# Optimization experiments

Measured on AMD Instinct MI355X. Metric: run time of the kernel, lower is better.

The kernel has to match this reference:

```python
import jax, jax.numpy as jnp
import numpy as np

D_MODEL = 1024
N_HEADS = 16
N_KV_HEADS = 4
HEAD_DIM = 64


def setup_inputs() -> dict:
    key = jax.random.key(0)
    ks = jax.random.split(key, 5)
    B, T, P = 2, 512, 8
    scale = 1.0 / np.sqrt(D_MODEL)
    return {
        "hidden_states": jax.random.normal(ks[0], (B, T, P, D_MODEL), dtype=jnp.float32),
        # weights stored [in, out] so y = x @ W (same math as nn.Linear with W^T)
        "Wq": jax.random.normal(ks[1], (D_MODEL, N_HEADS * HEAD_DIM), dtype=jnp.float32) * scale,
        "Wk": jax.random.normal(ks[2], (D_MODEL, N_KV_HEADS * HEAD_DIM), dtype=jnp.float32) * scale,
        "Wv": jax.random.normal(ks[3], (D_MODEL, N_KV_HEADS * HEAD_DIM), dtype=jnp.float32) * scale,
        "Wo": jax.random.normal(ks[4], (N_HEADS * HEAD_DIM, D_MODEL), dtype=jnp.float32) * scale,
    }


def _rope_tables(T, d):
    half = d // 2
    inv_freq = 1.0 / (10000.0 ** (jnp.arange(half, dtype=jnp.float32) / half))
    pos = jnp.arange(T, dtype=jnp.float32)
    angles = pos[:, None] * inv_freq[None, :]  # (T, half)
    return jnp.cos(angles), jnp.sin(angles)


def _apply_rope(x, cos, sin):
    # x: (B, P, T, H, d); cos/sin: (T, d/2)
    half = x.shape[-1] // 2
    x1, x2 = x[..., :half], x[..., half:]
    c = cos[None, None, :, None, :]
    s = sin[None, None, :, None, :]
    return jnp.concatenate([x1 * c - x2 * s, x1 * s + x2 * c], axis=-1)


def reference(hidden_states, Wq, Wk, Wv, Wo):
    B, T, P, _ = hidden_states.shape
    x = jnp.transpose(hidden_states, (0, 2, 1, 3))  # (B, P, T, C)
    q = (x @ Wq).reshape(B, P, T, N_HEADS, HEAD_DIM)
    k = (x @ Wk).reshape(B, P, T, N_KV_HEADS, HEAD_DIM)
    v = (x @ Wv).reshape(B, P, T, N_KV_HEADS, HEAD_DIM)

    rep = N_HEADS // N_KV_HEADS
    k = jnp.repeat(k, rep, axis=3)  # (B,P,T,H,d) interleaved like torch repeat/view
    v = jnp.repeat(v, rep, axis=3)

    cos, sin = _rope_tables(T, HEAD_DIM)
    q = _apply_rope(q, cos, sin)
    k = _apply_rope(k, cos, sin)

    # (B,P,H,T,d)
    q = jnp.transpose(q, (0, 1, 3, 2, 4))
    k = jnp.transpose(k, (0, 1, 3, 2, 4))
    v = jnp.transpose(v, (0, 1, 3, 2, 4))

    attn = jnp.einsum("bphqd,bphkd->bphqk", q, k) / jnp.sqrt(
        jnp.asarray(HEAD_DIM, q.dtype))
    attn = jax.nn.softmax(attn, axis=-1)
    out = jnp.einsum("bphqk,bphkd->bphqd", attn, v)
    out = jnp.transpose(out, (0, 1, 3, 2, 4)).reshape(B, P, T, N_HEADS * HEAD_DIM)
    out = jnp.transpose(out, (0, 2, 1, 3))  # (B, T, P, H*d)
    return out @ Wo
```

## Files before the change

kernel.cpp:

```cpp
#include <hip/hip_runtime.h>
#include <stdint.h>


typedef __attribute__((ext_vector_type(8))) short bf16x8;
typedef __attribute__((ext_vector_type(4))) float f32x4;
typedef __attribute__((ext_vector_type(16))) float f32x16;
typedef __attribute__((ext_vector_type(4))) unsigned short us4;
typedef __attribute__((ext_vector_type(8))) unsigned short us8;

static __device__ __forceinline__ unsigned short f2bf(float f) {
  unsigned u = __float_as_uint(f);
  u += 0x7fffu + ((u >> 16) & 1u);
  return (unsigned short)(u >> 16);
}
static __device__ __forceinline__ float bf2f(unsigned short s) {
  return __uint_as_float(((unsigned)s) << 16);
}

static __device__ __forceinline__ void ld_lds16(const void* g, void* l) {
  __builtin_amdgcn_global_load_lds(
      (const __attribute__((address_space(1))) void*)g,
      (__attribute__((address_space(3))) void*)l, 16, 0, 0);
}

static __device__ __forceinline__ f32x4 mfma16(bf16x8 a, bf16x8 b, f32x4 c) {
  return __builtin_amdgcn_mfma_f32_16x16x32_bf16(a, b, c, 0, 0, 0);
}
static __device__ __forceinline__ f32x16 mfma32(bf16x8 a, bf16x8 b, f32x16 c) {
  return __builtin_amdgcn_mfma_f32_32x32x16_bf16(a, b, c, 0, 0, 0);
}

__global__ __launch_bounds__(256) void conv_x(const float* __restrict__ hs,
                                              unsigned short* __restrict__ xb) {
  int gid = blockIdx.x * 256 + threadIdx.x;
  size_t e = (size_t)gid * 4;
  int r = (int)(e >> 10);
  int d = (int)(e & 1023);
  int b = r >> 12, p = (r >> 9) & 7, t = r & 511;
  const float4* src = (const float4*)(hs + ((((size_t)b * 512 + t) * 8 + p) << 10) + d);
  float4 v = *src;
  us4 o;
  o.x = f2bf(v.x); o.y = f2bf(v.y); o.z = f2bf(v.z); o.w = f2bf(v.w);
  *(us4*)(xb + e) = o;
}

__global__ __launch_bounds__(256) void conv_wt(const float* __restrict__ W,
                                               unsigned short* __restrict__ Wt, int N) {
  int gid = blockIdx.x * 256 + threadIdx.x;
  int c = gid & 1023;
  int n = gid >> 10;
  Wt[(size_t)n * 1024 + c] = f2bf(W[(size_t)c * N + n]);
}

template <int NT, int MODE>
__global__ __launch_bounds__(256) void gemm_bt(
    const unsigned short* __restrict__ A, const unsigned short* __restrict__ Bt,
    unsigned short* __restrict__ qb, unsigned short* __restrict__ kb,
    unsigned short* __restrict__ vtb, float* __restrict__ out) {
  constexpr int K = 1024;
  __shared__ __align__(16) unsigned short Sm[128 * 128];
  unsigned short* As = Sm;
  unsigned short* Bs = Sm + 128 * 64;
  unsigned short* Cs = Sm;

  int tid = threadIdx.x;
  int lane = tid & 63, wid = tid >> 6;
  int quad = lane >> 4, lo = lane & 15;
  int tn = blockIdx.x % NT, tm = blockIdx.x / NT;
  int wm = (wid >> 1) * 64, wn = (wid & 1) * 64;
  int srow = lane >> 3, schunk = lane & 7;

  f32x4 z = {0.f, 0.f, 0.f, 0.f};
  f32x4 acc[4][4];
  for (int i = 0; i < 4; ++i) for (int j = 0; j < 4; ++j) acc[i][j] = z;

  const unsigned short* Ab = A + (size_t)(tm * 128) * K;
  const unsigned short* Bb = Bt + (size_t)(tn * 128) * K;

  for (int k0 = 0; k0 < K; k0 += 64) {
    __syncthreads();
    for (int i = 0; i < 4; ++i) {
      int row = wid * 8 + i * 32 + srow;
      int cg = schunk ^ (row & 7);
      ld_lds16(Ab + (size_t)row * K + k0 + cg * 8, (char*)As + (wid * 8 + i * 32) * 128);
      ld_lds16(Bb + (size_t)row * K + k0 + cg * 8, (char*)Bs + (wid * 8 + i * 32) * 128);
    }
    __syncthreads();
#pragma unroll
    for (int kk = 0; kk < 64; kk += 32) {
      bf16x8 af[4], bb[4];
#pragma unroll
      for (int mi = 0; mi < 4; ++mi) {
        int row = wm + mi * 16 + lo;
        int cg = (quad + (kk >> 3)) ^ (row & 7);
        af[mi] = *(const bf16x8*)(As + (size_t)row * 64 + cg * 8);
      }
#pragma unroll
      for (int ni = 0; ni < 4; ++ni) {
        int row = wn + ni * 16 + lo;
        int cg = (quad + (kk >> 3)) ^ (row & 7);
        bb[ni] = *(const bf16x8*)(Bs + (size_t)row * 64 + cg * 8);
      }
#pragma unroll
      for (int mi = 0; mi < 4; ++mi)
#pragma unroll
        for (int ni = 0; ni < 4; ++ni)
          acc[mi][ni] = mfma16(af[mi], bb[ni], acc[mi][ni]);
    }
  }

  __syncthreads();

  if (MODE == 0 && tn < 10) {
    float qscale = (tn < 8) ? 0.125f : 1.0f;
#pragma unroll
    for (int mi = 0; mi < 4; ++mi)
#pragma unroll
      for (int r = 0; r < 4; ++r) {
        int t = (tm * 128 + wm + mi * 16 + quad * 4 + r) & 511;
#pragma unroll
        for (int ni = 0; ni < 2; ++ni) {
          float inv = exp2f((float)(ni * 16 + lo) * -0.41524101186092029f);
          float ang = (float)t * inv;
          float s, c;
          __sincosf(ang, &s, &c);
          float x1 = acc[mi][ni][r], x2 = acc[mi][ni + 2][r];
          acc[mi][ni][r]     = (x1 * c - x2 * s) * qscale;
          acc[mi][ni + 2][r] = (x1 * s + x2 * c) * qscale;
        }
      }
#pragma unroll
    for (int mi = 0; mi < 4; ++mi)
#pragma unroll
      for (int ni = 0; ni < 4; ++ni)
#pragma unroll
        for (int r = 0; r < 4; ++r) {
          int row = wm + mi * 16 + quad * 4 + r;
          int col = wn + ni * 16 + lo;
          int cs = col ^ (((row >> 2) & 3) << 3);
          Cs[row * 128 + cs] = f2bf(acc[mi][ni][r]);
        }
    __syncthreads();
    int tc = tid & 15, ro = tid >> 4;
#pragma unroll
    for (int it = 0; it < 8; ++it) {
      int row = ro + 16 * it;
      int cs = (tc * 8) ^ (((row >> 2) & 3) << 3);
      us8 v = *(const us8*)(Cs + row * 128 + cs);
      size_t grow = (size_t)(tm * 128 + row);
      if (tn < 8) {
        *(us8*)(qb + grow * 1024 + tn * 128 + tc * 8) = v;
      } else {
        *(us8*)(kb + grow * 256 + (tn - 8) * 128 + tc * 8) = v;
      }
    }
  } else {
    for (int mi = 0; mi < 4; ++mi) {
      for (int ni = 0; ni < 4; ++ni) {
        int col = tn * 128 + wn + ni * 16 + lo;
        for (int r = 0; r < 4; ++r) {
          int grow = tm * 128 + wm + mi * 16 + quad * 4 + r;
          float val = acc[mi][ni][r];
          if (MODE == 0) {
            int cc = col - 1280;
            int hh = cc >> 6, dd = cc & 63;
            int bp = grow >> 9, t = grow & 511;
            vtb[(((size_t)(bp * 4 + hh)) * 64 + dd) * 512 + t] = f2bf(val);
          } else {
            int bp = grow >> 9, t = grow & 511;
            int b = bp >> 3, p = bp & 7;
            out[((((size_t)b * 512 + t) * 8 + p) << 10) + col] = val;
          }
        }
      }
    }
  }
}

__global__ __launch_bounds__(256, 4) void attn(
    const unsigned short* __restrict__ qb, const unsigned short* __restrict__ kb,
    const unsigned short* __restrict__ vtb, unsigned short* __restrict__ ao) {
  __shared__ __align__(16) unsigned short Qs[128 * 64];
  __shared__ __align__(16) unsigned short Ks[64 * 64];
  __shared__ __align__(16) unsigned short Vs[64 * 64];

  int tid = threadIdx.x;
  int lane = tid & 63, wid = tid >> 6;
  int lo32 = lane & 31, hl = lane >> 5;
  int qt = blockIdx.x & 3, bph = blockIdx.x >> 2;
  int head = bph & 15, bp = bph >> 4;
  int kvh = head >> 2;
  int t0 = qt * 128;
  int srow = lane >> 3, schunk = lane & 7;

  const unsigned short* qg = qb + ((size_t)(bp * 512 + t0)) * 1024 + head * 64;
  const unsigned short* kg = kb + ((size_t)bp * 512) * 256 + kvh * 64;
  const unsigned short* vg = vtb + ((size_t)(bp * 4 + kvh)) * 64 * 512;

  for (int i = 0; i < 4; ++i) {
    int row = wid * 8 + i * 32 + srow;
    int cg = schunk ^ (row & 7);
    ld_lds16(qg + (size_t)row * 1024 + cg * 8, (char*)Qs + (wid * 8 + i * 32) * 128);
  }

  f32x16 z16 = {0.f};
  f32x16 o0 = z16, o1 = z16;
  float psum = 0.f;
  int qrow = wid * 32 + lo32;

  for (int kt = 0; kt < 512; kt += 64) {
    __syncthreads();
    for (int i = 0; i < 2; ++i) {
      int row = wid * 8 + i * 32 + srow;
      int cg = schunk ^ (row & 7);
      ld_lds16(kg + (size_t)(kt + row) * 256 + cg * 8, (char*)Ks + (wid * 8 + i * 32) * 128);
      ld_lds16(vg + (size_t)row * 512 + kt + cg * 8, (char*)Vs + (wid * 8 + i * 32) * 128);
    }
    __syncthreads();

    f32x16 st0 = z16, st1 = z16;
#pragma unroll
    for (int kkc = 0; kkc < 4; ++kkc) {
      int ch = 2 * kkc + hl;
      bf16x8 qf = *(const bf16x8*)(Qs + (size_t)qrow * 64 + ((ch ^ (qrow & 7)) * 8));
      bf16x8 kf0 = *(const bf16x8*)(Ks + (size_t)lo32 * 64 + ((ch ^ (lo32 & 7)) * 8));
      bf16x8 kf1 = *(const bf16x8*)(Ks + (size_t)(32 + lo32) * 64 + ((ch ^ (lo32 & 7)) * 8));
      st0 = mfma32(kf0, qf, st0);
      st1 = mfma32(kf1, qf, st1);
    }

#pragma unroll
    for (int t = 0; t < 2; ++t) {
      const f32x16& stv = t ? st1 : st0;
      unsigned pk[8], xpk[8];
#pragma unroll
      for (int p = 0; p < 8; ++p) {
        float e0 = __expf(stv[2 * p]);
        float e1 = __expf(stv[2 * p + 1]);
        psum += e0 + e1;
        pk[p] = ((__float_as_uint(e0) + 0x8000u) >> 16) |
                ((__float_as_uint(e1) + 0x8000u) & 0xffff0000u);
      }
#pragma unroll
      for (int p = 0; p < 8; ++p) xpk[p] = (unsigned)__shfl_xor((int)pk[p], 32);
#pragma unroll
      for (int cc = 0; cc < 2; ++cc) {
        int o = cc * 4;
        union { unsigned u[4]; bf16x8 v; } af;
        if (hl == 0) {
          af.u[0] = pk[o];      af.u[1] = pk[o + 1];
          af.u[2] = xpk[o];     af.u[3] = xpk[o + 1];
        } else {
          af.u[0] = xpk[o + 2]; af.u[1] = xpk[o + 3];
          af.u[2] = pk[o + 2];  af.u[3] = pk[o + 3];
        }
        int vch = 2 * (t * 2 + cc) + hl;
        bf16x8 v0 = *(const bf16x8*)(Vs + (size_t)lo32 * 64 + ((vch ^ (lo32 & 7)) * 8));
        bf16x8 v1 = *(const bf16x8*)(Vs + (size_t)(32 + lo32) * 64 + ((vch ^ (lo32 & 7)) * 8));
        o0 = mfma32(af.v, v0, o0);
        o1 = mfma32(af.v, v1, o1);
      }
    }
  }

  psum += __shfl_xor(psum, 32);
  float inv = 1.f / psum;
#pragma unroll
  for (int r = 0; r < 16; ++r) {
    int q_r = (r & 3) + 8 * (r >> 2) + 4 * hl;
    float sc = __shfl(inv, q_r);
    size_t grow = (size_t)(bp * 512 + t0 + wid * 32 + q_r);
    ao[grow * 1024 + head * 64 + lo32]      = f2bf(o0[r] * sc);
    ao[grow * 1024 + head * 64 + 32 + lo32] = f2bf(o1[r] * sc);
  }
}

extern "C" void kernel_launch(void* const* d_in, const int* in_sizes, int n_in,
                              void* d_out, int out_size, void* d_ws, size_t ws_size,
                              hipStream_t stream) {
  const float* hs = (const float*)d_in[0];
  const float* Wq = (const float*)d_in[1];
  const float* Wk = (const float*)d_in[2];
  const float* Wv = (const float*)d_in[3];
  const float* Wo = (const float*)d_in[4];
  float* out = (float*)d_out;

  unsigned short* xb   = (unsigned short*)d_ws;
  unsigned short* wqkv = xb + (size_t)8192 * 1024;
  unsigned short* wot  = wqkv + (size_t)1536 * 1024;
  unsigned short* qbuf = wot + (size_t)1024 * 1024;
  unsigned short* kbuf = qbuf + (size_t)8192 * 1024;
  unsigned short* vtb  = kbuf + (size_t)8192 * 256;
  unsigned short* ao   = xb;

  conv_x<<<8192, 256, 0, stream>>>(hs, xb);
  conv_wt<<<4096, 256, 0, stream>>>(Wq, wqkv, 1024);
  conv_wt<<<1024, 256, 0, stream>>>(Wk, wqkv + (size_t)1024 * 1024, 256);
  conv_wt<<<1024, 256, 0, stream>>>(Wv, wqkv + (size_t)1280 * 1024, 256);
  conv_wt<<<4096, 256, 0, stream>>>(Wo, wot, 1024);
  gemm_bt<12, 0><<<768, 256, 0, stream>>>(xb, wqkv, qbuf, kbuf, vtb, nullptr);
  attn<<<1024, 256, 0, stream>>>(qbuf, kbuf, vtb, ao);
  gemm_bt<8, 1><<<512, 256, 0, stream>>>(ao, wot, nullptr, nullptr, nullptr, out);
}
```

Before: 210.2 us.

## Fuse conversions with tiled weight transpose and register-prefetch GEMM loads

Merges the activation and four weight conversion kernels into one launch, and transposes weights through a padded LDS tile so global reads and writes are coalesced. The GEMM replaces direct global-to-LDS loads with register double buffering: the next K-slab is loaded into registers while the current slab is computed, then written to LDS. An occupancy hint is added to the GEMM's launch bounds. The register staging raises register pressure and adds explicit LDS stores.

```diff
diff --git a/kernel.cpp b/kernel.cpp
--- a/kernel.cpp
+++ b/kernel.cpp
@@ -13,9 +13,6 @@
   u += 0x7fffu + ((u >> 16) & 1u);
   return (unsigned short)(u >> 16);
 }
-static __device__ __forceinline__ float bf2f(unsigned short s) {
-  return __uint_as_float(((unsigned)s) << 16);
-}
 
 static __device__ __forceinline__ void ld_lds16(const void* g, void* l) {
   __builtin_amdgcn_global_load_lds(
@@ -30,30 +27,53 @@
   return __builtin_amdgcn_mfma_f32_32x32x16_bf16(a, b, c, 0, 0, 0);
 }
 
-__global__ __launch_bounds__(256) void conv_x(const float* __restrict__ hs,
-                                              unsigned short* __restrict__ xb) {
-  int gid = blockIdx.x * 256 + threadIdx.x;
-  size_t e = (size_t)gid * 4;
-  int r = (int)(e >> 10);
-  int d = (int)(e & 1023);
-  int b = r >> 12, p = (r >> 9) & 7, t = r & 511;
-  const float4* src = (const float4*)(hs + ((((size_t)b * 512 + t) * 8 + p) << 10) + d);
-  float4 v = *src;
-  us4 o;
-  o.x = f2bf(v.x); o.y = f2bf(v.y); o.z = f2bf(v.z); o.w = f2bf(v.w);
-  *(us4*)(xb + e) = o;
-}
-
-__global__ __launch_bounds__(256) void conv_wt(const float* __restrict__ W,
-                                               unsigned short* __restrict__ Wt, int N) {
-  int gid = blockIdx.x * 256 + threadIdx.x;
-  int c = gid & 1023;
-  int n = gid >> 10;
-  Wt[(size_t)n * 1024 + c] = f2bf(W[(size_t)c * N + n]);
+__global__ __launch_bounds__(256) void conv_all(
+    const float* __restrict__ hs, const float* __restrict__ Wq,
+    const float* __restrict__ Wk, const float* __restrict__ Wv,
+    const float* __restrict__ Wo, unsigned short* __restrict__ xb,
+    unsigned short* __restrict__ wqkv, unsigned short* __restrict__ wot) {
+  __shared__ float tile[64][65];
+  int bid = blockIdx.x, tid = threadIdx.x;
+  if (bid < 8192) {
+    int gid = bid * 256 + tid;
+    size_t e = (size_t)gid * 4;
+    int r = (int)(e >> 10);
+    int d = (int)(e & 1023);
+    int b = r >> 12, p = (r >> 9) & 7, t = r & 511;
+    const float4* src = (const float4*)(hs + ((((size_t)b * 512 + t) * 8 + p) << 10) + d);
+    float4 v = *src;
+    us4 o;
+    o.x = f2bf(v.x); o.y = f2bf(v.y); o.z = f2bf(v.z); o.w = f2bf(v.w);
+    *(us4*)(xb + e) = o;
+    return;
+  }
+  int tb = bid - 8192;
+  const float* W; unsigned short* Wt; int N, tc0, tn0;
+  if (tb < 256)      { W = Wq; Wt = wqkv;                       N = 1024; tc0 = (tb >> 4) * 64;          tn0 = (tb & 15) * 64; }
+  else if (tb < 320) { W = Wk; Wt = wqkv + (size_t)1024 * 1024; N = 256;  tc0 = ((tb - 256) >> 2) * 64;  tn0 = ((tb - 256) & 3) * 64; }
+  else if (tb < 384) { W = Wv; Wt = wqkv + (size_t)1280 * 1024; N = 256;  tc0 = ((tb - 320) >> 2) * 64;  tn0 = ((tb - 320) & 3) * 64; }
+  else               { W = Wo; Wt = wot;                        N = 1024; tc0 = ((tb - 384) >> 4) * 64;  tn0 = ((tb - 384) & 15) * 64; }
+  int tr = tid >> 4, tc = tid & 15;
+#pragma unroll
+  for (int i = 0; i < 4; ++i) {
+    int c = tr + i * 16;
+    float4 v = *(const float4*)(W + (size_t)(tc0 + c) * N + tn0 + tc * 4);
+    tile[c][tc * 4 + 0] = v.x; tile[c][tc * 4 + 1] = v.y;
+    tile[c][tc * 4 + 2] = v.z; tile[c][tc * 4 + 3] = v.w;
+  }
+  __syncthreads();
+#pragma unroll
+  for (int i = 0; i < 4; ++i) {
+    int n = tr + i * 16;
+    us4 o;
+    o.x = f2bf(tile[tc * 4 + 0][n]); o.y = f2bf(tile[tc * 4 + 1][n]);
+    o.z = f2bf(tile[tc * 4 + 2][n]); o.w = f2bf(tile[tc * 4 + 3][n]);
+    *(us4*)(Wt + (size_t)(tn0 + n) * 1024 + tc0 + tc * 4) = o;
+  }
 }
 
 template <int NT, int MODE>
-__global__ __launch_bounds__(256) void gemm_bt(
+__global__ __launch_bounds__(256, 3) void gemm_bt(
     const unsigned short* __restrict__ A, const unsigned short* __restrict__ Bt,
     unsigned short* __restrict__ qb, unsigned short* __restrict__ kb,
     unsigned short* __restrict__ vtb, float* __restrict__ out) {
@@ -74,32 +94,49 @@
   f32x4 acc[4][4];
   for (int i = 0; i < 4; ++i) for (int j = 0; j < 4; ++j) acc[i][j] = z;
 
-  const unsigned short* Ab = A + (size_t)(tm * 128) * K;
-  const unsigned short* Bb = Bt + (size_t)(tn * 128) * K;
+  int cg = schunk ^ srow;
+  const unsigned short* pa = A + ((size_t)(tm * 128) + wid * 8 + srow) * K + cg * 8;
+  const unsigned short* pb = Bt + ((size_t)(tn * 128) + wid * 8 + srow) * K + cg * 8;
+  unsigned short* wA = As + (size_t)(wid * 8 + srow * 0) * 0;
+  char* dA = (char*)As + (wid * 8) * 128 + lane * 16;
+  char* dB = (char*)Bs + (wid * 8) * 128 + lane * 16;
+
+  us8 ra[4], rb[4];
+#pragma unroll
+  for (int i = 0; i < 4; ++i) {
+    ra[i] = *(const us8*)(pa + (size_t)i * 32 * K);
+    rb[i] = *(const us8*)(pb + (size_t)i * 32 * K);
+  }
 
   for (int k0 = 0; k0 < K; k0 += 64) {
     __syncthreads();
+#pragma unroll
     for (int i = 0; i < 4; ++i) {
-      int row = wid * 8 + i * 32 + srow;
-      int cg = schunk ^ (row & 7);
-      ld_lds16(Ab + (size_t)row * K + k0 + cg * 8, (char*)As + (wid * 8 + i * 32) * 128);
-      ld_lds16(Bb + (size_t)row * K + k0 + cg * 8, (char*)Bs + (wid * 8 + i * 32) * 128);
-    }
-    __syncthreads();
+      *(us8*)(dA + i * 32 * 128) = ra[i];
+      *(us8*)(dB + i * 32 * 128) = rb[i];
+    }
+    __syncthreads();
+    if (k0 + 64 < K) {
+#pragma unroll
+      for (int i = 0; i < 4; ++i) {
+        ra[i] = *(const us8*)(pa + (size_t)i * 32 * K + k0 + 64);
+        rb[i] = *(const us8*)(pb + (size_t)i * 32 * K + k0 + 64);
+      }
+    }
 #pragma unroll
     for (int kk = 0; kk < 64; kk += 32) {
       bf16x8 af[4], bb[4];
 #pragma unroll
       for (int mi = 0; mi < 4; ++mi) {
         int row = wm + mi * 16 + lo;
-        int cg = (quad + (kk >> 3)) ^ (row & 7);
-        af[mi] = *(const bf16x8*)(As + (size_t)row * 64 + cg * 8);
+        int cgx = (quad + (kk >> 3)) ^ (row & 7);
+        af[mi] = *(const bf16x8*)(As + (size_t)row * 64 + cgx * 8);
       }
 #pragma unroll
       for (int ni = 0; ni < 4; ++ni) {
         int row = wn + ni * 16 + lo;
-        int cg = (quad + (kk >> 3)) ^ (row & 7);
-        bb[ni] = *(const bf16x8*)(Bs + (size_t)row * 64 + cg * 8);
+        int cgx = (quad + (kk >> 3)) ^ (row & 7);
+        bb[ni] = *(const bf16x8*)(Bs + (size_t)row * 64 + cgx * 8);
       }
 #pragma unroll
       for (int mi = 0; mi < 4; ++mi)
@@ -293,11 +330,7 @@
   unsigned short* vtb  = kbuf + (size_t)8192 * 256;
   unsigned short* ao   = xb;
 
-  conv_x<<<8192, 256, 0, stream>>>(hs, xb);
-  conv_wt<<<4096, 256, 0, stream>>>(Wq, wqkv, 1024);
-  conv_wt<<<1024, 256, 0, stream>>>(Wk, wqkv + (size_t)1024 * 1024, 256);
-  conv_wt<<<1024, 256, 0, stream>>>(Wv, wqkv + (size_t)1280 * 1024, 256);
-  conv_wt<<<4096, 256, 0, stream>>>(Wo, wot, 1024);
+  conv_all<<<8832, 256, 0, stream>>>(hs, Wq, Wk, Wv, Wo, xb, wqkv, wot);
   gemm_bt<12, 0><<<768, 256, 0, stream>>>(xb, wqkv, qbuf, kbuf, vtb, nullptr);
   attn<<<1024, 256, 0, stream>>>(qbuf, kbuf, vtb, ao);
   gemm_bt<8, 1><<<512, 256, 0, stream>>>(ao, wot, nullptr, nullptr, nullptr, out);
```

Result: faster. 176.3 us (-16.1%).
